# Kernel optimization log

Hardware: AMD Instinct MI355X
Metric: run time of the kernel (lower is better)

## Reference

```python
import jax, jax.numpy as jnp
import numpy as np

N_NODES = 50000
N_EDGES = 800000
D = 128


def setup_inputs() -> dict:
    key = jax.random.key(0)
    ks = jax.random.split(key, 8)
    x = jax.random.normal(ks[0], (N_NODES, D), dtype=jnp.float32)
    src = jax.random.randint(ks[1], (N_EDGES,), 0, N_NODES, dtype=jnp.int64)
    dst = jax.random.randint(ks[2], (N_EDGES,), 0, N_NODES, dtype=jnp.int64)
    edge_weights = jax.random.uniform(ks[3], (N_EDGES,), dtype=jnp.float32)
    scale = 1.0 / np.sqrt(D)
    W1 = jax.random.normal(ks[4], (D, D), dtype=jnp.float32) * scale
    b1 = jnp.zeros((D,), dtype=jnp.float32)
    W2 = jax.random.normal(ks[5], (D, D), dtype=jnp.float32) * scale
    b2 = jnp.zeros((D,), dtype=jnp.float32)
    return {"x": x, "src": src, "dst": dst, "edge_weights": edge_weights,
            "W1": W1, "b1": b1, "W2": W2, "b2": b2}


def reference(x, src, dst, edge_weights, W1, b1, W2, b2):
    n_nodes = x.shape[0]
    # out-degrees (edges where node is the source), clamped to >= 1
    deg = jax.ops.segment_sum(jnp.ones_like(src, dtype=x.dtype), src,
                              num_segments=n_nodes)
    deg = jnp.maximum(deg, 1.0)
    # per-edge symmetric-normalization coefficient: 1/sqrt(deg_u * deg_v)
    coef = jax.lax.rsqrt(deg[src] * deg[dst]) * edge_weights  # [E]
    # gather-multiply-scatter: sum_{u->v} x[u] * coef into node v
    msgs = x[src] * coef[:, None]                              # [E, D]
    agg = jax.ops.segment_sum(msgs, dst, num_segments=n_nodes)  # [N, D]
    # FFN: Linear -> ReLU -> Linear (dropout = 0)
    h = jax.nn.relu(agg @ W1 + b1)
    return h @ W2 + b2
```

## Files before the change

kernel.cpp:

```cpp
#include <hip/hip_runtime.h>

#define NN 50000
#define NE 800000
#define D  128
#define HB 128
#define CH 6272
#define PW 50176
#define XB 128
#define RB2 98

typedef short short8 __attribute__((ext_vector_type(8)));
typedef float f32x4  __attribute__((ext_vector_type(4)));
typedef unsigned char u8;

__device__ __forceinline__ ushort f2bf(float f) {
    union { float f; unsigned u; } v; v.f = f;
    unsigned r = v.u + 0x7FFFu + ((v.u >> 16) & 1u);
    return (ushort)(r >> 16);
}


__global__ __launch_bounds__(1024) void prep_kernel(const int* __restrict__ src,
                                                    const int* __restrict__ dst,
                                                    const float* __restrict__ x,
                                                    const float* __restrict__ W1,
                                                    const float* __restrict__ W2,
                                                    u8* __restrict__ psrc,
                                                    u8* __restrict__ pdst,
                                                    ushort* __restrict__ xbf,
                                                    ushort* __restrict__ W1t,
                                                    ushort* __restrict__ W2t) {
    __shared__ unsigned bins[2 * PW / 4];
    const int t = threadIdx.x, b = blockIdx.x;

    if (b < HB) {
        for (int i = t; i < 2 * PW / 16; i += 1024)
            ((uint4*)bins)[i] = make_uint4(0, 0, 0, 0);
        __syncthreads();
        const int base = b * CH;
#pragma unroll
        for (int i = 0; i < 2; ++i) {
            int e0 = base + i * 4096 + t * 4;
            if (e0 < base + CH && e0 < NE) {
                int4 s4 = *(const int4*)(src + e0);
                int4 d4 = *(const int4*)(dst + e0);
                atomicAdd(&bins[s4.x >> 2], 1u << ((s4.x & 3) << 3));
                atomicAdd(&bins[s4.y >> 2], 1u << ((s4.y & 3) << 3));
                atomicAdd(&bins[s4.z >> 2], 1u << ((s4.z & 3) << 3));
                atomicAdd(&bins[s4.w >> 2], 1u << ((s4.w & 3) << 3));
                atomicAdd(&bins[PW / 4 + (d4.x >> 2)], 1u << ((d4.x & 3) << 3));
                atomicAdd(&bins[PW / 4 + (d4.y >> 2)], 1u << ((d4.y & 3) << 3));
                atomicAdd(&bins[PW / 4 + (d4.z >> 2)], 1u << ((d4.z & 3) << 3));
                atomicAdd(&bins[PW / 4 + (d4.w >> 2)], 1u << ((d4.w & 3) << 3));
            }
        }
        __syncthreads();
        uint4* os = (uint4*)(psrc + (size_t)b * PW);
        uint4* od = (uint4*)(pdst + (size_t)b * PW);
        for (int i = t; i < PW / 16; i += 1024) {
            os[i] = ((const uint4*)bins)[i];
            od[i] = ((const uint4*)(bins + PW / 4))[i];
        }
    } else if (b < HB + 4) {
        int c = (b - HB) * 1024 + t;
        if (c < 4096) {
            const float* W = (c < 2048) ? W1 : W2;
            ushort* Wt     = (c < 2048) ? W1t : W2t;
            int cc = c & 2047;
            int n  = cc >> 4;
            int k0 = (cc & 15) * 8;
            ushort tmp[8];
#pragma unroll
            for (int j = 0; j < 8; ++j) tmp[j] = f2bf(W[(k0 + j) * D + n]);
            *reinterpret_cast<uint4*>(Wt + n * D + k0) = *reinterpret_cast<uint4*>(tmp);
        }
    } else {
        for (int i = (b - HB - 4) * 1024 + t; i < NN * D / 8; i += XB * 1024) {
            const float4* p = (const float4*)(x + (size_t)i * 8);
            float4 v0 = p[0], v1 = p[1];
            ushort tmp[8];
            tmp[0] = f2bf(v0.x); tmp[1] = f2bf(v0.y); tmp[2] = f2bf(v0.z); tmp[3] = f2bf(v0.w);
            tmp[4] = f2bf(v1.x); tmp[5] = f2bf(v1.y); tmp[6] = f2bf(v1.z); tmp[7] = f2bf(v1.w);
            *reinterpret_cast<uint4*>(xbf + (size_t)i * 8) = *reinterpret_cast<uint4*>(tmp);
        }
    }
}

__global__ __launch_bounds__(256) void xprep_kernel(const float* __restrict__ x,
                                                    ushort* __restrict__ xbf) {
    int i = blockIdx.x * 256 + threadIdx.x;
    if (i >= NN * D / 8) return;
    const float4* p = (const float4*)(x + (size_t)i * 8);
    float4 v0 = p[0], v1 = p[1];
    ushort tmp[8];
    tmp[0] = f2bf(v0.x); tmp[1] = f2bf(v0.y); tmp[2] = f2bf(v0.z); tmp[3] = f2bf(v0.w);
    tmp[4] = f2bf(v1.x); tmp[5] = f2bf(v1.y); tmp[6] = f2bf(v1.z); tmp[7] = f2bf(v1.w);
    *reinterpret_cast<uint4*>(xbf + (size_t)i * 8) = *reinterpret_cast<uint4*>(tmp);
}


__global__ __launch_bounds__(1024) void reduce_kernel(const unsigned* __restrict__ psrc32,
                                                      unsigned* __restrict__ pdst32,
                                                      float* __restrict__ rsq,
                                                      int* __restrict__ cnt,
                                                      int* __restrict__ bsum98) {
    __shared__ int sm[128];
    const int t = threadIdx.x;
    const int g = (blockIdx.x * 1024 + t) >> 3;
    const int c = t & 7;
    const size_t stride = PW / 4;

    unsigned wv[16];
#pragma unroll
    for (int i = 0; i < 16; ++i)
        wv[i] = pdst32[(size_t)(c * 16 + i) * stride + g];
    unsigned t02 = 0, t13 = 0;
#pragma unroll
    for (int i = 0; i < 16; ++i) {
        t02 += wv[i] & 0x00FF00FFu;
        t13 += (wv[i] >> 8) & 0x00FF00FFu;
    }
    unsigned p02 = 0, p13 = 0;
#pragma unroll
    for (int i = 0; i < 16; ++i) {
        unsigned w = psrc32[(size_t)(c * 16 + i) * stride + g];
        p02 += w & 0x00FF00FFu;
        p13 += (w >> 8) & 0x00FF00FFu;
    }
    unsigned i02 = t02, i13 = t13;
#pragma unroll
    for (int off = 1; off < 8; off <<= 1) {
        unsigned v02 = __shfl_up(i02, off, 8);
        unsigned v13 = __shfl_up(i13, off, 8);
        if (c >= off) { i02 += v02; i13 += v13; }
    }
    unsigned q02 = p02, q13 = p13, u02 = t02, u13 = t13;
#pragma unroll
    for (int off = 1; off < 8; off <<= 1) {
        q02 += __shfl_xor(q02, off, 8);
        q13 += __shfl_xor(q13, off, 8);
        u02 += __shfl_xor(u02, off, 8);
        u13 += __shfl_xor(u13, off, 8);
    }
    unsigned r02 = i02 - t02, r13 = i13 - t13;
#pragma unroll
    for (int i = 0; i < 16; ++i) {
        unsigned w = wv[i];
        pdst32[(size_t)(c * 16 + i) * stride + g] =
            (r02 & 0xFFu) | ((r13 & 0xFFu) << 8) |
            (r02 & 0x00FF0000u) | ((r13 & 0x00FF0000u) << 8);
        r02 += w & 0x00FF00FFu;
        r13 += (w >> 8) & 0x00FF00FFu;
    }
    if (c == 0) {
        int v0 = g * 4;
        int dg_[4] = { (int)(q02 & 0xFFFFu), (int)(q13 & 0xFFFFu),
                       (int)(q02 >> 16),     (int)(q13 >> 16) };
        int ct_[4] = { (int)(u02 & 0xFFFFu), (int)(u13 & 0xFFFFu),
                       (int)(u02 >> 16),     (int)(u13 >> 16) };
        if (v0 + 3 < NN) {
            *(float4*)(rsq + v0) = make_float4(rsqrtf(fmaxf((float)dg_[0], 1.f)),
                                               rsqrtf(fmaxf((float)dg_[1], 1.f)),
                                               rsqrtf(fmaxf((float)dg_[2], 1.f)),
                                               rsqrtf(fmaxf((float)dg_[3], 1.f)));
            *(int4*)(cnt + v0) = make_int4(ct_[0], ct_[1], ct_[2], ct_[3]);
        } else {
            for (int j = 0; j < 4; ++j)
                if (v0 + j < NN) {
                    rsq[v0 + j] = rsqrtf(fmaxf((float)dg_[j], 1.f));
                    cnt[v0 + j] = ct_[j];
                }
        }
        sm[t >> 3] = ct_[0] + ct_[1] + ct_[2] + ct_[3];
    }
    __syncthreads();
    for (int s = 64; s > 0; s >>= 1) {
        if (t < s) sm[t] += sm[t + s];
        __syncthreads();
    }
    if (t == 0) bsum98[blockIdx.x] = sm[0];
}


__global__ __launch_bounds__(512) void scan_write(const int* __restrict__ cnt,
                                                  const int* __restrict__ bsum98,
                                                  int* __restrict__ offs) {
    __shared__ int sm[512];
    const int b = blockIdx.x, t = threadIdx.x;
    sm[t] = (t < RB2 && t < b) ? bsum98[t] : 0;
    __syncthreads();
    for (int s = 256; s > 0; s >>= 1) {
        if (t < s) sm[t] += sm[t + s];
        __syncthreads();
    }
    int base = sm[0];
    __syncthreads();
    int i = b * 512 + t;
    int v = (i < NN) ? cnt[i] : 0;
    sm[t] = v;
    __syncthreads();
    for (int d2 = 1; d2 < 512; d2 <<= 1) {
        int u = (t >= d2) ? sm[t - d2] : 0;
        __syncthreads();
        sm[t] += u;
        __syncthreads();
    }
    if (i < NN) offs[i] = base + sm[t] - v;
    if (b == 0 && t == 0) offs[NN] = NE;
}


__global__ __launch_bounds__(1024) void scatter_kernel(const int* __restrict__ src,
                                                       const int* __restrict__ dst,
                                                       const float* __restrict__ ew,
                                                       const float* __restrict__ rsq,
                                                       const int* __restrict__ offs,
                                                       const u8* __restrict__ pd,
                                                       unsigned* __restrict__ csr) {
    __shared__ unsigned cur[PW / 4];
    const int t = threadIdx.x, b = blockIdx.x;
    for (int i = t; i < PW / 16; i += 1024)
        ((uint4*)cur)[i] = make_uint4(0, 0, 0, 0);
    __syncthreads();

    const u8* pdrow = pd + (size_t)b * PW;
    const int base = b * CH;
#pragma unroll
    for (int i = 0; i < 2; ++i) {
        int e0 = base + i * 4096 + t * 4;
        if (e0 < base + CH && e0 < NE) {
            int4 s4 = *(const int4*)(src + e0);
            int4 d4 = *(const int4*)(dst + e0);
            float4 w4 = *(const float4*)(ew + e0);
#pragma unroll
            for (int j = 0; j < 4; ++j) {
                int s = (j == 0) ? s4.x : (j == 1) ? s4.y : (j == 2) ? s4.z : s4.w;
                int d = (j == 0) ? d4.x : (j == 1) ? d4.y : (j == 2) ? d4.z : d4.w;
                float w = (j == 0) ? w4.x : (j == 1) ? w4.y : (j == 2) ? w4.z : w4.w;
                int sh = (d & 3) << 3;
                unsigned old = atomicAdd(&cur[d >> 2], 1u << sh);
                int rel = (int)((old >> sh) & 0xFFu);
                int pos = offs[d] + (int)pdrow[d] + rel;
                float coef = rsq[s] * rsq[d] * w;
                csr[pos] = (unsigned)s | ((unsigned)f2bf(coef) << 16);
            }
        }
    }
}


__device__ __forceinline__ void acc_row(unsigned e, int lane,
                                        const ushort* __restrict__ xbf,
                                        float& a0, float& a1, float& a2, float& a3) {
    float c = __int_as_float(e & 0xFFFF0000u);
    uint2 u = ((const uint2*)(xbf + (size_t)(e & 0xFFFFu) * D))[lane];
    a0 = fmaf(__int_as_float((int)(u.x << 16)),        c, a0);
    a1 = fmaf(__int_as_float((int)(u.x & 0xFFFF0000u)), c, a1);
    a2 = fmaf(__int_as_float((int)(u.y << 16)),        c, a2);
    a3 = fmaf(__int_as_float((int)(u.y & 0xFFFF0000u)), c, a3);
}

__global__ __launch_bounds__(256) void gather_bf16_kernel(const int* __restrict__ offs,
                                                          const unsigned* __restrict__ csr,
                                                          const ushort* __restrict__ xbf,
                                                          float* __restrict__ agg) {
    int v = blockIdx.x * 8 + (threadIdx.x >> 5);
    if (v >= NN) return;
    int lane = threadIdx.x & 31;
    int beg = offs[v], end = offs[v + 1];
    float a0 = 0.f, a1 = 0.f, a2 = 0.f, a3 = 0.f;
    for (int i0 = beg; i0 < end; i0 += 32) {
        int n = end - i0; if (n > 32) n = 32;
        unsigned ej = (lane < n) ? csr[i0 + lane] : 0u;
        int j = 0;
        for (; j + 3 < n; j += 4) {
            unsigned e0 = __shfl(ej, j,     32);
            unsigned e1 = __shfl(ej, j + 1, 32);
            unsigned e2 = __shfl(ej, j + 2, 32);
            unsigned e3 = __shfl(ej, j + 3, 32);
            uint2 u0 = ((const uint2*)(xbf + (size_t)(e0 & 0xFFFFu) * D))[lane];
            uint2 u1 = ((const uint2*)(xbf + (size_t)(e1 & 0xFFFFu) * D))[lane];
            uint2 u2 = ((const uint2*)(xbf + (size_t)(e2 & 0xFFFFu) * D))[lane];
            uint2 u3 = ((const uint2*)(xbf + (size_t)(e3 & 0xFFFFu) * D))[lane];
            float c0 = __int_as_float(e0 & 0xFFFF0000u);
            float c1 = __int_as_float(e1 & 0xFFFF0000u);
            float c2 = __int_as_float(e2 & 0xFFFF0000u);
            float c3 = __int_as_float(e3 & 0xFFFF0000u);
            a0 = fmaf(__int_as_float((int)(u0.x << 16)),         c0, a0);
            a1 = fmaf(__int_as_float((int)(u0.x & 0xFFFF0000u)), c0, a1);
            a2 = fmaf(__int_as_float((int)(u0.y << 16)),         c0, a2);
            a3 = fmaf(__int_as_float((int)(u0.y & 0xFFFF0000u)), c0, a3);
            a0 = fmaf(__int_as_float((int)(u1.x << 16)),         c1, a0);
            a1 = fmaf(__int_as_float((int)(u1.x & 0xFFFF0000u)), c1, a1);
            a2 = fmaf(__int_as_float((int)(u1.y << 16)),         c1, a2);
            a3 = fmaf(__int_as_float((int)(u1.y & 0xFFFF0000u)), c1, a3);
            a0 = fmaf(__int_as_float((int)(u2.x << 16)),         c2, a0);
            a1 = fmaf(__int_as_float((int)(u2.x & 0xFFFF0000u)), c2, a1);
            a2 = fmaf(__int_as_float((int)(u2.y << 16)),         c2, a2);
            a3 = fmaf(__int_as_float((int)(u2.y & 0xFFFF0000u)), c2, a3);
            a0 = fmaf(__int_as_float((int)(u3.x << 16)),         c3, a0);
            a1 = fmaf(__int_as_float((int)(u3.x & 0xFFFF0000u)), c3, a1);
            a2 = fmaf(__int_as_float((int)(u3.y << 16)),         c3, a2);
            a3 = fmaf(__int_as_float((int)(u3.y & 0xFFFF0000u)), c3, a3);
        }
        for (; j < n; ++j) {
            unsigned e = __shfl(ej, j, 32);
            acc_row(e, lane, xbf, a0, a1, a2, a3);
        }
    }
    ((float4*)(agg + (size_t)v * D))[lane] = make_float4(a0, a1, a2, a3);
}


__global__ __launch_bounds__(256) void ffn_mfma_kernel(const float* __restrict__ agg,
                                                       const ushort* __restrict__ W1t,
                                                       const ushort* __restrict__ W2t,
                                                       const float* __restrict__ b1,
                                                       const float* __restrict__ b2,
                                                       float* __restrict__ out) {
    __shared__ ushort Wt[128 * 128];
    __shared__ ushort hS[4][16 * 128];

    const int t  = threadIdx.x;
    const int w  = t >> 6;
    const int l  = t & 63;
    const int lr = l & 15;
    const int lk = l >> 4;
    const int r0 = blockIdx.x * 64;

    for (int i = 0; i < 8; ++i) {
        int c = i * 256 + t;
        int n = c >> 4;
        int slot = c & 15;
        uint4 v = ((const uint4*)W1t)[c];
        int byte = n * 256 + ((slot * 16) ^ ((n & 7) << 4));
        *(uint4*)((char*)Wt + byte) = v;
    }

    const int arow = r0 + w * 16 + lr;
    short8 afrag[4];
#pragma unroll
    for (int kb = 0; kb < 4; ++kb) {
        int k = kb * 32 + lk * 8;
        float4 v0 = make_float4(0.f, 0.f, 0.f, 0.f), v1 = v0;
        if (arow < NN) {
            const float4* ap = (const float4*)(agg + (size_t)arow * D + k);
            v0 = ap[0]; v1 = ap[1];
        }
        short8 a;
        a[0] = (short)f2bf(v0.x); a[1] = (short)f2bf(v0.y);
        a[2] = (short)f2bf(v0.z); a[3] = (short)f2bf(v0.w);
        a[4] = (short)f2bf(v1.x); a[5] = (short)f2bf(v1.y);
        a[6] = (short)f2bf(v1.z); a[7] = (short)f2bf(v1.w);
        afrag[kb] = a;
    }
    __syncthreads();

    f32x4 acc[8];
#pragma unroll
    for (int nt = 0; nt < 8; ++nt) acc[nt] = (f32x4){0.f, 0.f, 0.f, 0.f};
#pragma unroll
    for (int kb = 0; kb < 4; ++kb) {
        int kbyte = (kb * 32 + lk * 8) * 2;
#pragma unroll
        for (int nt = 0; nt < 8; ++nt) {
            int n = nt * 16 + lr;
            short8 b = *(const short8*)((const char*)Wt + n * 256 + (kbyte ^ ((n & 7) << 4)));
            acc[nt] = __builtin_amdgcn_mfma_f32_16x16x32_bf16(afrag[kb], b, acc[nt], 0, 0, 0);
        }
    }
#pragma unroll
    for (int nt = 0; nt < 8; ++nt) {
        int col = nt * 16 + lr;
        float bb = b1[col];
#pragma unroll
        for (int r = 0; r < 4; ++r) {
            int row = lk * 4 + r;
            float h = fmaxf(acc[nt][r] + bb, 0.0f);
            int byte = row * 256 + ((col * 2) ^ ((row & 7) << 4));
            *(ushort*)((char*)&hS[w][0] + byte) = f2bf(h);
        }
    }
    __syncthreads();

    for (int i = 0; i < 8; ++i) {
        int c = i * 256 + t;
        int n = c >> 4;
        int slot = c & 15;
        uint4 v = ((const uint4*)W2t)[c];
        int byte = n * 256 + ((slot * 16) ^ ((n & 7) << 4));
        *(uint4*)((char*)Wt + byte) = v;
    }
    __syncthreads();

    short8 hfrag[4];
#pragma unroll
    for (int kb = 0; kb < 4; ++kb) {
        int kbyte = (kb * 32 + lk * 8) * 2;
        hfrag[kb] = *(const short8*)((const char*)&hS[w][0] + lr * 256 + (kbyte ^ ((lr & 7) << 4)));
    }
#pragma unroll
    for (int nt = 0; nt < 8; ++nt) acc[nt] = (f32x4){0.f, 0.f, 0.f, 0.f};
#pragma unroll
    for (int kb = 0; kb < 4; ++kb) {
        int kbyte = (kb * 32 + lk * 8) * 2;
#pragma unroll
        for (int nt = 0; nt < 8; ++nt) {
            int n = nt * 16 + lr;
            short8 b = *(const short8*)((const char*)Wt + n * 256 + (kbyte ^ ((n & 7) << 4)));
            acc[nt] = __builtin_amdgcn_mfma_f32_16x16x32_bf16(hfrag[kb], b, acc[nt], 0, 0, 0);
        }
    }
#pragma unroll
    for (int nt = 0; nt < 8; ++nt) {
        int col = nt * 16 + lr;
        float bb = b2[col];
#pragma unroll
        for (int r = 0; r < 4; ++r) {
            int row = r0 + w * 16 + lk * 4 + r;
            if (row < NN) out[(size_t)row * D + col] = acc[nt][r] + bb;
        }
    }
}


extern "C" void kernel_launch(void* const* d_in, const int* in_sizes, int n_in,
                              void* d_out, int out_size, void* d_ws, size_t ws_size,
                              hipStream_t stream) {
    const float* x  = (const float*)d_in[0];
    const int* src  = (const int*)d_in[1];
    const int* dst  = (const int*)d_in[2];
    const float* ew = (const float*)d_in[3];
    const float* W1 = (const float*)d_in[4];
    const float* b1 = (const float*)d_in[5];
    const float* W2 = (const float*)d_in[6];
    const float* b2 = (const float*)d_in[7];
    float* out = (float*)d_out;

    char* base = (char*)d_ws;
    size_t off = 0;
    auto alloc = [&](size_t bytes) { char* p = base + off; off = (off + bytes + 15) & ~(size_t)15; return p; };
    u8* psrc      = (u8*)alloc((size_t)HB * PW);
    u8* pdst      = (u8*)alloc((size_t)HB * PW);
    float* rsq    = (float*)alloc((size_t)NN * 4);
    int* cnt      = (int*)alloc((size_t)NN * 4);
    int* offs     = (int*)alloc((size_t)(NN + 1) * 4);
    int* bsum98   = (int*)alloc((size_t)RB2 * 4);
    unsigned* csr = (unsigned*)alloc((size_t)NE * 4);
    ushort* W1t   = (ushort*)alloc((size_t)D * D * 2);
    ushort* W2t   = (ushort*)alloc((size_t)D * D * 2);
    ushort* xbf_own = (ushort*)alloc((size_t)NN * D * 2);
    bool own_xbf = ws_size >= off;
    ushort* xbf = own_xbf ? xbf_own : (ushort*)psrc;

    int prep_grid = own_xbf ? (HB + 4 + XB) : (HB + 4);
    prep_kernel<<<prep_grid, 1024, 0, stream>>>(src, dst, x, W1, W2,
                                                psrc, pdst, xbf, W1t, W2t);
    reduce_kernel<<<RB2, 1024, 0, stream>>>((const unsigned*)psrc, (unsigned*)pdst,
                                            rsq, cnt, bsum98);
    scan_write<<<RB2, 512, 0, stream>>>(cnt, bsum98, offs);
    scatter_kernel<<<HB, 1024, 0, stream>>>(src, dst, ew, rsq, offs, pdst, csr);
    if (!own_xbf)
        xprep_kernel<<<(NN * D / 8 + 255) / 256, 256, 0, stream>>>(x, xbf);
    gather_bf16_kernel<<<(NN + 7) / 8, 256, 0, stream>>>(offs, csr, xbf, out);
    ffn_mfma_kernel<<<(NN + 63) / 64, 256, 0, stream>>>(out, W1t, W2t, b1, b2, out);
}
```

Measured before the change: 131.4 us.

## Double histogram blocks, fold x conversion into them, store aggregate as bf16

Histogram blocks go from 128 to 256, each handling half as many edges. Each block also converts a slice of x to bf16, replacing the separate conversion blocks. The reduce kernel uses 16-lane groups over 196 blocks, and the scan and scatter are adjusted to match. The gather now writes the aggregate as bf16 into its own buffer, which the FFN reads directly without converting, halving intermediate traffic. In exchange the reduce reads twice as many per-block partial histograms, the workspace needs an extra bf16 buffer, and the fallback for a small workspace is removed.

New measurement: 123.8 us. 5.8% less time.

```diff
diff --git a/kernel.cpp b/kernel.cpp
--- a/kernel.cpp
+++ b/kernel.cpp
@@ -3,11 +3,12 @@
 #define NN 50000
 #define NE 800000
 #define D  128
-#define HB 128
-#define CH 6272
+#define HB 256
+#define CH 3136
 #define PW 50176
-#define XB 128
-#define RB2 98
+#define REDB 196
+#define SCB 98
+#define XCHUNK 3125
 
 typedef short short8 __attribute__((ext_vector_type(8)));
 typedef float f32x4  __attribute__((ext_vector_type(4)));
@@ -38,21 +39,18 @@
             ((uint4*)bins)[i] = make_uint4(0, 0, 0, 0);
         __syncthreads();
         const int base = b * CH;
-#pragma unroll
-        for (int i = 0; i < 2; ++i) {
-            int e0 = base + i * 4096 + t * 4;
-            if (e0 < base + CH && e0 < NE) {
-                int4 s4 = *(const int4*)(src + e0);
-                int4 d4 = *(const int4*)(dst + e0);
-                atomicAdd(&bins[s4.x >> 2], 1u << ((s4.x & 3) << 3));
-                atomicAdd(&bins[s4.y >> 2], 1u << ((s4.y & 3) << 3));
-                atomicAdd(&bins[s4.z >> 2], 1u << ((s4.z & 3) << 3));
-                atomicAdd(&bins[s4.w >> 2], 1u << ((s4.w & 3) << 3));
-                atomicAdd(&bins[PW / 4 + (d4.x >> 2)], 1u << ((d4.x & 3) << 3));
-                atomicAdd(&bins[PW / 4 + (d4.y >> 2)], 1u << ((d4.y & 3) << 3));
-                atomicAdd(&bins[PW / 4 + (d4.z >> 2)], 1u << ((d4.z & 3) << 3));
-                atomicAdd(&bins[PW / 4 + (d4.w >> 2)], 1u << ((d4.w & 3) << 3));
-            }
+        int e0 = base + t * 4;
+        if (e0 < base + CH && e0 < NE) {
+            int4 s4 = *(const int4*)(src + e0);
+            int4 d4 = *(const int4*)(dst + e0);
+            atomicAdd(&bins[s4.x >> 2], 1u << ((s4.x & 3) << 3));
+            atomicAdd(&bins[s4.y >> 2], 1u << ((s4.y & 3) << 3));
+            atomicAdd(&bins[s4.z >> 2], 1u << ((s4.z & 3) << 3));
+            atomicAdd(&bins[s4.w >> 2], 1u << ((s4.w & 3) << 3));
+            atomicAdd(&bins[PW / 4 + (d4.x >> 2)], 1u << ((d4.x & 3) << 3));
+            atomicAdd(&bins[PW / 4 + (d4.y >> 2)], 1u << ((d4.y & 3) << 3));
+            atomicAdd(&bins[PW / 4 + (d4.z >> 2)], 1u << ((d4.z & 3) << 3));
+            atomicAdd(&bins[PW / 4 + (d4.w >> 2)], 1u << ((d4.w & 3) << 3));
         }
         __syncthreads();
         uint4* os = (uint4*)(psrc + (size_t)b * PW);
@@ -61,7 +59,16 @@
             os[i] = ((const uint4*)bins)[i];
             od[i] = ((const uint4*)(bins + PW / 4))[i];
         }
-    } else if (b < HB + 4) {
+        const int xbase = b * XCHUNK;
+        for (int i = xbase + t; i < xbase + XCHUNK; i += 1024) {
+            const float4* p = (const float4*)(x + (size_t)i * 8);
+            float4 v0 = p[0], v1 = p[1];
+            ushort tmp[8];
+            tmp[0] = f2bf(v0.x); tmp[1] = f2bf(v0.y); tmp[2] = f2bf(v0.z); tmp[3] = f2bf(v0.w);
+            tmp[4] = f2bf(v1.x); tmp[5] = f2bf(v1.y); tmp[6] = f2bf(v1.z); tmp[7] = f2bf(v1.w);
+            *reinterpret_cast<uint4*>(xbf + (size_t)i * 8) = *reinterpret_cast<uint4*>(tmp);
+        }
+    } else {
         int c = (b - HB) * 1024 + t;
         if (c < 4096) {
             const float* W = (c < 2048) ? W1 : W2;
@@ -74,28 +81,7 @@
             for (int j = 0; j < 8; ++j) tmp[j] = f2bf(W[(k0 + j) * D + n]);
             *reinterpret_cast<uint4*>(Wt + n * D + k0) = *reinterpret_cast<uint4*>(tmp);
         }
-    } else {
-        for (int i = (b - HB - 4) * 1024 + t; i < NN * D / 8; i += XB * 1024) {
-            const float4* p = (const float4*)(x + (size_t)i * 8);
-            float4 v0 = p[0], v1 = p[1];
-            ushort tmp[8];
-            tmp[0] = f2bf(v0.x); tmp[1] = f2bf(v0.y); tmp[2] = f2bf(v0.z); tmp[3] = f2bf(v0.w);
-            tmp[4] = f2bf(v1.x); tmp[5] = f2bf(v1.y); tmp[6] = f2bf(v1.z); tmp[7] = f2bf(v1.w);
-            *reinterpret_cast<uint4*>(xbf + (size_t)i * 8) = *reinterpret_cast<uint4*>(tmp);
-        }
-    }
-}
-
-__global__ __launch_bounds__(256) void xprep_kernel(const float* __restrict__ x,
-                                                    ushort* __restrict__ xbf) {
-    int i = blockIdx.x * 256 + threadIdx.x;
-    if (i >= NN * D / 8) return;
-    const float4* p = (const float4*)(x + (size_t)i * 8);
-    float4 v0 = p[0], v1 = p[1];
-    ushort tmp[8];
-    tmp[0] = f2bf(v0.x); tmp[1] = f2bf(v0.y); tmp[2] = f2bf(v0.z); tmp[3] = f2bf(v0.w);
-    tmp[4] = f2bf(v1.x); tmp[5] = f2bf(v1.y); tmp[6] = f2bf(v1.z); tmp[7] = f2bf(v1.w);
-    *reinterpret_cast<uint4*>(xbf + (size_t)i * 8) = *reinterpret_cast<uint4*>(tmp);
+    }
 }
 
 
@@ -103,11 +89,11 @@
                                                       unsigned* __restrict__ pdst32,
                                                       float* __restrict__ rsq,
                                                       int* __restrict__ cnt,
-                                                      int* __restrict__ bsum98) {
-    __shared__ int sm[128];
+                                                      int* __restrict__ bsum196) {
+    __shared__ int sm[64];
     const int t = threadIdx.x;
-    const int g = (blockIdx.x * 1024 + t) >> 3;
-    const int c = t & 7;
+    const int g = (blockIdx.x * 1024 + t) >> 4;
+    const int c = t & 15;
     const size_t stride = PW / 4;
 
     unsigned wv[16];
@@ -129,18 +115,18 @@
     }
     unsigned i02 = t02, i13 = t13;
 #pragma unroll
-    for (int off = 1; off < 8; off <<= 1) {
-        unsigned v02 = __shfl_up(i02, off, 8);
-        unsigned v13 = __shfl_up(i13, off, 8);
+    for (int off = 1; off < 16; off <<= 1) {
+        unsigned v02 = __shfl_up(i02, off, 16);
+        unsigned v13 = __shfl_up(i13, off, 16);
         if (c >= off) { i02 += v02; i13 += v13; }
     }
     unsigned q02 = p02, q13 = p13, u02 = t02, u13 = t13;
 #pragma unroll
-    for (int off = 1; off < 8; off <<= 1) {
-        q02 += __shfl_xor(q02, off, 8);
-        q13 += __shfl_xor(q13, off, 8);
-        u02 += __shfl_xor(u02, off, 8);
-        u13 += __shfl_xor(u13, off, 8);
+    for (int off = 1; off < 16; off <<= 1) {
+        q02 += __shfl_xor(q02, off, 16);
+        q13 += __shfl_xor(q13, off, 16);
+        u02 += __shfl_xor(u02, off, 16);
+        u13 += __shfl_xor(u13, off, 16);
     }
     unsigned r02 = i02 - t02, r13 = i13 - t13;
 #pragma unroll
@@ -171,23 +157,23 @@
                     cnt[v0 + j] = ct_[j];
                 }
         }
-        sm[t >> 3] = ct_[0] + ct_[1] + ct_[2] + ct_[3];
-    }
-    __syncthreads();
-    for (int s = 64; s > 0; s >>= 1) {
+        sm[t >> 4] = ct_[0] + ct_[1] + ct_[2] + ct_[3];
+    }
+    __syncthreads();
+    for (int s = 32; s > 0; s >>= 1) {
         if (t < s) sm[t] += sm[t + s];
         __syncthreads();
     }
-    if (t == 0) bsum98[blockIdx.x] = sm[0];
+    if (t == 0) bsum196[blockIdx.x] = sm[0];
 }
 
 
 __global__ __launch_bounds__(512) void scan_write(const int* __restrict__ cnt,
-                                                  const int* __restrict__ bsum98,
+                                                  const int* __restrict__ bsum196,
                                                   int* __restrict__ offs) {
     __shared__ int sm[512];
     const int b = blockIdx.x, t = threadIdx.x;
-    sm[t] = (t < RB2 && t < b) ? bsum98[t] : 0;
+    sm[t] = (t < REDB && t < 2 * b) ? bsum196[t] : 0;
     __syncthreads();
     for (int s = 256; s > 0; s >>= 1) {
         if (t < s) sm[t] += sm[t + s];
@@ -225,25 +211,22 @@
 
     const u8* pdrow = pd + (size_t)b * PW;
     const int base = b * CH;
-#pragma unroll
-    for (int i = 0; i < 2; ++i) {
-        int e0 = base + i * 4096 + t * 4;
-        if (e0 < base + CH && e0 < NE) {
-            int4 s4 = *(const int4*)(src + e0);
-            int4 d4 = *(const int4*)(dst + e0);
-            float4 w4 = *(const float4*)(ew + e0);
-#pragma unroll
-            for (int j = 0; j < 4; ++j) {
-                int s = (j == 0) ? s4.x : (j == 1) ? s4.y : (j == 2) ? s4.z : s4.w;
-                int d = (j == 0) ? d4.x : (j == 1) ? d4.y : (j == 2) ? d4.z : d4.w;
-                float w = (j == 0) ? w4.x : (j == 1) ? w4.y : (j == 2) ? w4.z : w4.w;
-                int sh = (d & 3) << 3;
-                unsigned old = atomicAdd(&cur[d >> 2], 1u << sh);
-                int rel = (int)((old >> sh) & 0xFFu);
-                int pos = offs[d] + (int)pdrow[d] + rel;
-                float coef = rsq[s] * rsq[d] * w;
-                csr[pos] = (unsigned)s | ((unsigned)f2bf(coef) << 16);
-            }
+    int e0 = base + t * 4;
+    if (e0 < base + CH && e0 < NE) {
+        int4 s4 = *(const int4*)(src + e0);
+        int4 d4 = *(const int4*)(dst + e0);
+        float4 w4 = *(const float4*)(ew + e0);
+#pragma unroll
+        for (int j = 0; j < 4; ++j) {
+            int s = (j == 0) ? s4.x : (j == 1) ? s4.y : (j == 2) ? s4.z : s4.w;
+            int d = (j == 0) ? d4.x : (j == 1) ? d4.y : (j == 2) ? d4.z : d4.w;
+            float w = (j == 0) ? w4.x : (j == 1) ? w4.y : (j == 2) ? w4.z : w4.w;
+            int sh = (d & 3) << 3;
+            unsigned old = atomicAdd(&cur[d >> 2], 1u << sh);
+            int rel = (int)((old >> sh) & 0xFFu);
+            int pos = offs[d] + (int)pdrow[d] + rel;
+            float coef = rsq[s] * rsq[d] * w;
+            csr[pos] = (unsigned)s | ((unsigned)f2bf(coef) << 16);
         }
     }
 }
@@ -263,7 +246,7 @@
 __global__ __launch_bounds__(256) void gather_bf16_kernel(const int* __restrict__ offs,
                                                           const unsigned* __restrict__ csr,
                                                           const ushort* __restrict__ xbf,
-                                                          float* __restrict__ agg) {
+                                                          ushort* __restrict__ aggbf) {
     int v = blockIdx.x * 8 + (threadIdx.x >> 5);
     if (v >= NN) return;
     int lane = threadIdx.x & 31;
@@ -308,11 +291,13 @@
             acc_row(e, lane, xbf, a0, a1, a2, a3);
         }
     }
-    ((float4*)(agg + (size_t)v * D))[lane] = make_float4(a0, a1, a2, a3);
-}
-
-
-__global__ __launch_bounds__(256) void ffn_mfma_kernel(const float* __restrict__ agg,
+    unsigned lo = (unsigned)f2bf(a0) | ((unsigned)f2bf(a1) << 16);
+    unsigned hi = (unsigned)f2bf(a2) | ((unsigned)f2bf(a3) << 16);
+    ((uint2*)(aggbf + (size_t)v * D))[lane] = make_uint2(lo, hi);
+}
+
+
+__global__ __launch_bounds__(256) void ffn_mfma_kernel(const ushort* __restrict__ aggbf,
                                                        const ushort* __restrict__ W1t,
                                                        const ushort* __restrict__ W2t,
                                                        const float* __restrict__ b1,
@@ -338,22 +323,11 @@
     }
 
     const int arow = r0 + w * 16 + lr;
+    const ushort* ap = aggbf + (size_t)arow * D;
     short8 afrag[4];
 #pragma unroll
-    for (int kb = 0; kb < 4; ++kb) {
-        int k = kb * 32 + lk * 8;
-        float4 v0 = make_float4(0.f, 0.f, 0.f, 0.f), v1 = v0;
-        if (arow < NN) {
-            const float4* ap = (const float4*)(agg + (size_t)arow * D + k);
-            v0 = ap[0]; v1 = ap[1];
-        }
-        short8 a;
-        a[0] = (short)f2bf(v0.x); a[1] = (short)f2bf(v0.y);
-        a[2] = (short)f2bf(v0.z); a[3] = (short)f2bf(v0.w);
-        a[4] = (short)f2bf(v1.x); a[5] = (short)f2bf(v1.y);
-        a[6] = (short)f2bf(v1.z); a[7] = (short)f2bf(v1.w);
-        afrag[kb] = a;
-    }
+    for (int kb = 0; kb < 4; ++kb)
+        afrag[kb] = *(const short8*)(ap + kb * 32 + lk * 8);
     __syncthreads();
 
     f32x4 acc[8];
@@ -440,28 +414,24 @@
     char* base = (char*)d_ws;
     size_t off = 0;
     auto alloc = [&](size_t bytes) { char* p = base + off; off = (off + bytes + 15) & ~(size_t)15; return p; };
-    u8* psrc      = (u8*)alloc((size_t)HB * PW);
-    u8* pdst      = (u8*)alloc((size_t)HB * PW);
-    float* rsq    = (float*)alloc((size_t)NN * 4);
-    int* cnt      = (int*)alloc((size_t)NN * 4);
-    int* offs     = (int*)alloc((size_t)(NN + 1) * 4);
-    int* bsum98   = (int*)alloc((size_t)RB2 * 4);
-    unsigned* csr = (unsigned*)alloc((size_t)NE * 4);
-    ushort* W1t   = (ushort*)alloc((size_t)D * D * 2);
-    ushort* W2t   = (ushort*)alloc((size_t)D * D * 2);
-    ushort* xbf_own = (ushort*)alloc((size_t)NN * D * 2);
-    bool own_xbf = ws_size >= off;
-    ushort* xbf = own_xbf ? xbf_own : (ushort*)psrc;
-
-    int prep_grid = own_xbf ? (HB + 4 + XB) : (HB + 4);
-    prep_kernel<<<prep_grid, 1024, 0, stream>>>(src, dst, x, W1, W2,
-                                                psrc, pdst, xbf, W1t, W2t);
-    reduce_kernel<<<RB2, 1024, 0, stream>>>((const unsigned*)psrc, (unsigned*)pdst,
-                                            rsq, cnt, bsum98);
-    scan_write<<<RB2, 512, 0, stream>>>(cnt, bsum98, offs);
+    u8* psrc       = (u8*)alloc((size_t)HB * PW);
+    u8* pdst       = (u8*)alloc((size_t)HB * PW);
+    float* rsq     = (float*)alloc((size_t)NN * 4);
+    int* cnt       = (int*)alloc((size_t)NN * 4);
+    int* offs      = (int*)alloc((size_t)(NN + 1) * 4);
+    int* bsum196   = (int*)alloc((size_t)REDB * 4);
+    unsigned* csr  = (unsigned*)alloc((size_t)NE * 4);
+    ushort* W1t    = (ushort*)alloc((size_t)D * D * 2);
+    ushort* W2t    = (ushort*)alloc((size_t)D * D * 2);
+    ushort* xbf    = (ushort*)alloc((size_t)NN * D * 2);
+    ushort* aggbf  = (ushort*)alloc((size_t)(NN + 64) * D * 2);
+
+    prep_kernel<<<HB + 4, 1024, 0, stream>>>(src, dst, x, W1, W2,
+                                             psrc, pdst, xbf, W1t, W2t);
+    reduce_kernel<<<REDB, 1024, 0, stream>>>((const unsigned*)psrc, (unsigned*)pdst,
+                                             rsq, cnt, bsum196);
+    scan_write<<<SCB, 512, 0, stream>>>(cnt, bsum196, offs);
     scatter_kernel<<<HB, 1024, 0, stream>>>(src, dst, ew, rsq, offs, pdst, csr);
-    if (!own_xbf)
-        xprep_kernel<<<(NN * D / 8 + 255) / 256, 256, 0, stream>>>(x, xbf);
-    gather_bf16_kernel<<<(NN + 7) / 8, 256, 0, stream>>>(offs, csr, xbf, out);
-    ffn_mfma_kernel<<<(NN + 63) / 64, 256, 0, stream>>>(out, W1t, W2t, b1, b2, out);
-}
+    gather_bf16_kernel<<<(NN + 7) / 8, 256, 0, stream>>>(offs, csr, xbf, aggbf);
+    ffn_mfma_kernel<<<(NN + 63) / 64, 256, 0, stream>>>(aggbf, W1t, W2t, b1, b2, out);
+}
```
